# Performance work log

Hardware: AMD Instinct MI355X
Metric: run time of the kernel (lower is better)

## Reference

```python
import jax, jax.numpy as jnp
import numpy as np

N, P, D, FDIM, TFEAT = 65536, 6, 256, 8, 16
RAW_DIM = 4 + TFEAT  # 20
IN_DIM = 3 + FDIM + 3 + 3  # xyz + frame embedding + rigid xyz + viewdir = 17


def setup_inputs() -> dict:
    key = jax.random.key(0)
    ks = jax.random.split(key, 16)
    inp = {
        "tpts": jax.random.normal(ks[0], (N, P, 3), jnp.float32),
        "bigpts": jax.random.normal(ks[1], (N, P, 3), jnp.float32),
        "viewdir": jax.random.normal(ks[2], (N, P, 3), jnp.float32),
        "dists": jax.random.uniform(ks[3], (N,), jnp.float32),
        "part_dist": jax.random.uniform(ks[4], (1, N, P), jnp.float32),
        "frame_dim": jax.random.normal(ks[5], (FDIM,), jnp.float32),
        "W1": jax.random.normal(ks[6], (P, IN_DIM, D), jnp.float32) / np.sqrt(IN_DIM),
        "b1": jax.random.normal(ks[7], (P, D), jnp.float32) * 0.01,
        "W2": jax.random.normal(ks[8], (P, D, D), jnp.float32) / np.sqrt(D),
        "b2": jax.random.normal(ks[9], (P, D), jnp.float32) * 0.01,
        "W3": jax.random.normal(ks[10], (P, D, RAW_DIM), jnp.float32) / np.sqrt(D),
        "b3": jax.random.normal(ks[11], (P, RAW_DIM), jnp.float32) * 0.01,
        "Wocc": jax.random.normal(ks[12], (P, D, 1), jnp.float32) / np.sqrt(D),
        "bocc": jax.random.normal(ks[13], (P, 1), jnp.float32) * 0.01,
        "tflag": jax.random.randint(ks[14], (N, P), 0, 2).astype(bool),
    }
    return inp


def _part_mlps(tpts, bigpts, viewdir, frame_dim, W1, b1, W2, b2, W3, b3, Wocc, bocc):
    # Run all P part networks on all N points (batched per-part GEMMs).
    n = tpts.shape[0]
    frame = jnp.broadcast_to(frame_dim, (n, P, FDIM))
    x = jnp.concatenate([tpts, frame, bigpts, viewdir], axis=-1)  # (N,P,17)
    h = jax.nn.relu(jnp.einsum('npi,pid->npd', x, W1) + b1)
    h = jax.nn.relu(jnp.einsum('npd,pde->npe', h, W2) + b2)
    raw_p = jnp.einsum('npd,pdr->npr', h, W3) + b3               # (N,P,20)
    occ_p = jax.nn.sigmoid(jnp.einsum('npd,pdo->npo', h, Wocc) + bocc)  # (N,P,1)
    return raw_p, occ_p


def reference(tpts, bigpts, viewdir, dists, part_dist, frame_dim,
              W1, b1, W2, b2, W3, b3, Wocc, bocc, tflag):
    raw_p, occ_p = _part_mlps(tpts, bigpts, viewdir, frame_dim,
                              W1, b1, W2, b2, W3, b3, Wocc, bocc)
    # scatter-back equivalent: unflagged (point, part) slots stay zero
    flag = tflag[..., None].astype(raw_p.dtype)  # (N,P,1)
    raws = raw_p * flag                           # (N,P,20)
    occs = occ_p * flag                           # (N,P,1)
    # cfg.aggr == 'mean'
    raw = raws.mean(axis=1)                       # (N,20)
    occ = occs.mean(axis=1)                       # (N,1)
    tocc = occs[..., 0]                           # (N,P)
    return jnp.concatenate([raw, occ, tocc], axis=-1)  # (N, 20+1+P)
```

## Files before the change

kernel.cpp:

```cpp
#include <hip/hip_runtime.h>
#include <hip/hip_bf16.h>

using bf16 = __hip_bfloat16;
typedef __bf16 bf16x8 __attribute__((ext_vector_type(8)));
typedef __bf16 bf16x4v __attribute__((ext_vector_type(4)));
typedef float f32x4 __attribute__((ext_vector_type(4)));
typedef float f32x16 __attribute__((ext_vector_type(16)));

#define MFMA32(a, b, c) __builtin_amdgcn_mfma_f32_32x32x16_bf16((a), (b), (c), 0, 0, 0)

__device__ __forceinline__ void bar_lds() {
  asm volatile("s_waitcnt lgkmcnt(0)" ::: "memory");
  __builtin_amdgcn_s_barrier();
}


__global__ void prep_kernel(const float* __restrict__ W1, const float* __restrict__ b1,
                            const float* __restrict__ W2, const float* __restrict__ W3,
                            const float* __restrict__ Wocc, __bf16* __restrict__ ws) {
  const int b = blockIdx.x;
  const int tid = threadIdx.x;
  if (b < 96) {
    __shared__ float tile[64][65];
    const int p = b >> 4, t = b & 15;
    const int d0 = (t >> 2) * 64, e0 = (t & 3) * 64;
    const int lane = tid & 63, grp = tid >> 6;
    const float* src = W2 + p * 65536 + (d0 + grp * 16) * 256 + e0 + lane;
#pragma unroll
    for (int i = 0; i < 16; ++i) tile[grp * 16 + i][lane] = src[i * 256];
    __syncthreads();
#pragma unroll
    for (int q = 0; q < 2; ++q) {
      const int m = tid + q * 256;
      const int ee = m >> 3, c = m & 7;
      bf16x8 v;
#pragma unroll
      for (int j = 0; j < 8; ++j) v[j] = (__bf16)tile[c * 8 + j][ee];
      *reinterpret_cast<bf16x8*>(
          &ws[49152 + p * 65536 + (e0 + ee) * 256 + d0 + c * 8]) = v;
    }
    return;
  }
  const int t = 49152 + (b - 96) * 256 + tid;
  if (t < 55296) {
    const int u = t - 49152;
    const int p = u >> 10, r = u & 1023, n = r >> 2, c = r & 3;
    bf16x8 v;
#pragma unroll
    for (int j = 0; j < 8; ++j) {
      const int k = c * 8 + j;
      float x = 0.f;
      if (k < 17) {
        const int ko = (k < 8) ? k + 3 : ((k < 11) ? k - 8 : k);
        x = W1[p * 4352 + ko * 256 + n];
      } else if (k == 17) {
        x = b1[p * 256 + n];
      }
      v[j] = (__bf16)x;
    }
    *reinterpret_cast<bf16x8*>(&ws[p * 8192 + n * 32 + c * 8]) = v;
  } else if (t < 61440) {
    const int u = t - 55296;
    const int p = u >> 10, r = u & 1023, row = r >> 5, c = r & 31;
    bf16x8 v;
#pragma unroll
    for (int j = 0; j < 8; ++j) {
      const int k = c * 8 + j;
      float x = 0.f;
      if (row < 20)       x = W3[p * 5120 + k * 20 + row];
      else if (row == 20) x = Wocc[p * 256 + k];
      v[j] = (__bf16)x;
    }
    *reinterpret_cast<bf16x8*>(&ws[442368 + p * 8192 + row * 256 + c * 8]) = v;
  }
}

__global__ __launch_bounds__(256, 2) void tpose_main(
    const float* __restrict__ tpts, const float* __restrict__ bigpts,
    const float* __restrict__ viewdir, const float* __restrict__ frame,
    const float* __restrict__ b2g, const float* __restrict__ b3g,
    const float* __restrict__ boccg, const int* __restrict__ tflag,
    const __bf16* __restrict__ ws, float* __restrict__ out) {
  const __bf16* __restrict__ W1t = ws;
  const __bf16* __restrict__ W2t = ws + 49152;
  const __bf16* __restrict__ W3t = ws + 442368;

  __shared__ __align__(16) __bf16 Xf[128 * 40];
  __shared__ __align__(16) __bf16 Hf[128 * 256];
  __shared__ float Tocc[128 * 6];

  const int tid = threadIdx.x;
  const int w = tid >> 6;
  const int lane = tid & 63;
  const int ln5 = lane & 31;
  const int hi = lane >> 5;
  const int e5 = ln5 & 7;
  const int n0 = blockIdx.x * 128;
  const int ptD = w * 32 + ln5;

  if (tid < 128) {
    bf16x8 f8;
#pragma unroll
    for (int j = 0; j < 8; ++j) f8[j] = (__bf16)frame[j];
    *reinterpret_cast<bf16x8*>(&Xf[tid * 40]) = f8;
    bf16x8 z = {};
    z[1] = (__bf16)1.0f;
    *reinterpret_cast<bf16x8*>(&Xf[tid * 40 + 16]) = z;
    bf16x8 z2 = {};
    *reinterpret_cast<bf16x8*>(&Xf[tid * 40 + 24]) = z2;
  }

  const int role = tid & 3;
  const float* __restrict__ dynsrc =
      (role == 0) ? tpts : (role == 1) ? bigpts : viewdir;

  float pre[2][3];
#pragma unroll
  for (int pass = 0; pass < 2; ++pass) {
    const int pt = (tid >> 2) + pass * 64;
    const int base3 = (n0 + pt) * 18;
#pragma unroll
    for (int i = 0; i < 3; ++i) pre[pass][i] = dynsrc[base3 + i];
  }
  float flv = (tflag[(n0 + ptD) * 6] != 0) ? 1.f : 0.f;

  float psum[12];
#pragma unroll
  for (int k = 0; k < 12; ++k) psum[k] = 0.f;

  for (int p = 0; p < 6; ++p) {
    if (role < 3) {
#pragma unroll
      for (int pass = 0; pass < 2; ++pass) {
        const int pt = (tid >> 2) + pass * 64;
#pragma unroll
        for (int i = 0; i < 3; ++i)
          Xf[pt * 40 + 8 + role * 3 + i] = (__bf16)pre[pass][i];
      }
    }

    bf16x8 aw[2][2];
#pragma unroll
    for (int mt = 0; mt < 2; ++mt)
#pragma unroll
      for (int kt = 0; kt < 2; ++kt)
        aw[mt][kt] = *reinterpret_cast<const bf16x8*>(
            &W1t[p * 8192 + (w * 64 + mt * 32 + ln5) * 32 + kt * 16 + hi * 8]);

    bar_lds();

    f32x16 acc[2][4];
#pragma unroll
    for (int mt = 0; mt < 2; ++mt)
#pragma unroll
      for (int nt = 0; nt < 4; ++nt)
#pragma unroll
        for (int k = 0; k < 16; ++k) acc[mt][nt][k] = 0.f;
#pragma unroll
    for (int nt = 0; nt < 4; ++nt)
#pragma unroll
      for (int kt = 0; kt < 2; ++kt) {
        const bf16x8 xb = *reinterpret_cast<const bf16x8*>(
            &Xf[(nt * 32 + ln5) * 40 + kt * 16 + hi * 8]);
#pragma unroll
        for (int mt = 0; mt < 2; ++mt)
          acc[mt][nt] = MFMA32(aw[mt][kt], xb, acc[mt][nt]);
      }
#pragma unroll
    for (int mt = 0; mt < 2; ++mt)
#pragma unroll
      for (int q = 0; q < 4; ++q) {
        const int off = (((w * 8 + mt * 4 + q) ^ e5) << 3) + hi * 4;
#pragma unroll
        for (int nt = 0; nt < 4; ++nt) {
          bf16x4v hv;
#pragma unroll
          for (int r = 0; r < 4; ++r)
            hv[r] = (__bf16)fmaxf(acc[mt][nt][q * 4 + r], 0.f);
          *reinterpret_cast<bf16x4v*>(&Hf[(nt * 32 + ln5) * 256 + off]) = hv;
        }
      }

    bar_lds();

    const __bf16* __restrict__ w2p =
        W2t + p * 65536 + (w * 64 + ln5) * 256 + hi * 8;
    bf16x8 a2[2];
#pragma unroll
    for (int mt = 0; mt < 2; ++mt)
      a2[mt] = *reinterpret_cast<const bf16x8*>(w2p + mt * 8192);
    f32x4 b2q[2][4];
#pragma unroll
    for (int mt = 0; mt < 2; ++mt)
#pragma unroll
      for (int q = 0; q < 4; ++q)
        b2q[mt][q] = *reinterpret_cast<const f32x4*>(
            &b2g[p * 256 + w * 64 + mt * 32 + q * 8 + hi * 4]);

    const int pn = (p < 5) ? p + 1 : 5;
#pragma unroll
    for (int pass = 0; pass < 2; ++pass) {
      const int pt = (tid >> 2) + pass * 64;
      const int base3 = ((n0 + pt) * 6 + pn) * 3;
#pragma unroll
      for (int i = 0; i < 3; ++i) pre[pass][i] = dynsrc[base3 + i];
    }
    const float fln = (tflag[(n0 + ptD) * 6 + pn] != 0) ? 1.f : 0.f;

#pragma unroll
    for (int mt = 0; mt < 2; ++mt)
#pragma unroll
      for (int nt = 0; nt < 4; ++nt)
#pragma unroll
        for (int q = 0; q < 4; ++q)
#pragma unroll
          for (int r = 0; r < 4; ++r)
            acc[mt][nt][q * 4 + r] = b2q[mt][q][r];

    __builtin_amdgcn_s_setprio(1);
#pragma unroll 1
    for (int kt = 0; kt < 16; ++kt) {
      bf16x8 a2n[2];
      if (kt < 15) {
#pragma unroll
        for (int mt = 0; mt < 2; ++mt)
          a2n[mt] = *reinterpret_cast<const bf16x8*>(
              w2p + mt * 8192 + (kt + 1) * 16);
      }
      const int off = ((kt * 2 + hi) ^ e5) << 3;
      bf16x8 hb[4];
#pragma unroll
      for (int nt = 0; nt < 4; ++nt)
        hb[nt] = *reinterpret_cast<const bf16x8*>(
            &Hf[(nt * 32 + ln5) * 256 + off]);
#pragma unroll
      for (int nt = 0; nt < 4; ++nt)
#pragma unroll
        for (int mt = 0; mt < 2; ++mt)
          acc[mt][nt] = MFMA32(a2[mt], hb[nt], acc[mt][nt]);
#pragma unroll
      for (int mt = 0; mt < 2; ++mt) a2[mt] = a2n[mt];
    }
    __builtin_amdgcn_s_setprio(0);

    bar_lds();

#pragma unroll
    for (int mt = 0; mt < 2; ++mt)
#pragma unroll
      for (int q = 0; q < 4; ++q) {
        const int off = (((w * 8 + mt * 4 + q) ^ e5) << 3) + hi * 4;
#pragma unroll
        for (int nt = 0; nt < 4; ++nt) {
          bf16x4v hv;
#pragma unroll
          for (int r = 0; r < 4; ++r)
            hv[r] = (__bf16)fmaxf(acc[mt][nt][q * 4 + r], 0.f);
          *reinterpret_cast<bf16x4v*>(&Hf[(nt * 32 + ln5) * 256 + off]) = hv;
        }
      }

    bar_lds();

    f32x16 acc3;
#pragma unroll
    for (int q = 0; q < 4; ++q)
#pragma unroll
      for (int r = 0; r < 4; ++r) {
        const int d = q * 8 + hi * 4 + r;
        float v = 0.f;
        if (d < 20)       v = b3g[p * 20 + d];
        else if (d == 20) v = boccg[p];
        acc3[q * 4 + r] = v;
      }
    const __bf16* __restrict__ w3p = W3t + p * 8192 + ln5 * 256 + hi * 8;
#pragma unroll 4
    for (int kt = 0; kt < 16; ++kt) {
      const bf16x8 a3 = *reinterpret_cast<const bf16x8*>(w3p + kt * 16);
      const bf16x8 hb = *reinterpret_cast<const bf16x8*>(
          &Hf[ptD * 256 + (((kt * 2 + hi) ^ e5) << 3)]);
      acc3 = MFMA32(a3, hb, acc3);
    }

#pragma unroll
    for (int k = 0; k < 12; ++k) {
      const int d = (k >> 2) * 8 + hi * 4 + (k & 3);
      if (d < 20) {
        psum[k] += flv * acc3[k];
      } else if (d == 20) {
        const float occ = 1.f / (1.f + __expf(-acc3[k]));
        Tocc[ptD * 6 + p] = flv * occ;
        psum[k] += flv * occ;
      }
    }

    flv = fln;
  }

  bar_lds();
  float* stage = reinterpret_cast<float*>(Hf);
  const float inv6 = 1.f / 6.f;
#pragma unroll
  for (int k = 0; k < 12; ++k) {
    const int d = (k >> 2) * 8 + hi * 4 + (k & 3);
    if (d <= 20) stage[ptD * 27 + d] = psum[k] * inv6;
  }
  if (tid < 128) {
#pragma unroll
    for (int pp = 0; pp < 6; ++pp) stage[tid * 27 + 21 + pp] = Tocc[tid * 6 + pp];
  }
  bar_lds();
  float* outp = out + (size_t)n0 * 27;
#pragma unroll
  for (int q = 0; q < 4; ++q) {
    const int m = tid + q * 256;
    if (m < 864)
      *reinterpret_cast<f32x4*>(&outp[m * 4]) =
          *reinterpret_cast<const f32x4*>(&stage[m * 4]);
  }
}

extern "C" void kernel_launch(void* const* d_in, const int* in_sizes, int n_in,
                              void* d_out, int out_size, void* d_ws, size_t ws_size,
                              hipStream_t stream) {
  const float* tpts    = (const float*)d_in[0];
  const float* bigpts  = (const float*)d_in[1];
  const float* viewdir = (const float*)d_in[2];
  const float* frame   = (const float*)d_in[5];
  const float* W1      = (const float*)d_in[6];
  const float* b1      = (const float*)d_in[7];
  const float* W2      = (const float*)d_in[8];
  const float* b2      = (const float*)d_in[9];
  const float* W3      = (const float*)d_in[10];
  const float* b3      = (const float*)d_in[11];
  const float* Wocc    = (const float*)d_in[12];
  const float* bocc    = (const float*)d_in[13];
  const int*   tflag   = (const int*)d_in[14];
  __bf16* ws  = (__bf16*)d_ws;
  float*  out = (float*)d_out;

  prep_kernel<<<144, 256, 0, stream>>>(W1, b1, W2, W3, Wocc, ws);
  tpose_main<<<512, 256, 0, stream>>>(tpts, bigpts, viewdir, frame, b2, b3,
                                      bocc, tflag, ws, out);
}
```

Baseline: 183.8 us.

## Repartition layer-2 GEMM so each wave owns its points across all output features

Layer 2 is reorganized so each wave computes all 256 output features for its own 32 points, instead of a 64-feature slice for all 128 points. Each wave now reads only its own rows of H from LDS and streams W2 fragments from global memory in a rotating register buffer. Because every wave writes and reads only its own H rows, the two block-wide barriers around layer 2 and layer 3 can become a local LDS wait. The cost is four times more W2 global/L2 traffic per wave and a larger accumulator set (8 tiles), which raises register pressure.

```diff
diff --git a/kernel.cpp b/kernel.cpp
--- a/kernel.cpp
+++ b/kernel.cpp
@@ -128,6 +128,8 @@
 #pragma unroll
   for (int k = 0; k < 12; ++k) psum[k] = 0.f;
 
+  f32x16 acc[8];
+
   for (int p = 0; p < 6; ++p) {
     if (role < 3) {
 #pragma unroll
@@ -149,13 +151,10 @@
 
     bar_lds();
 
-    f32x16 acc[2][4];
-#pragma unroll
-    for (int mt = 0; mt < 2; ++mt)
-#pragma unroll
-      for (int nt = 0; nt < 4; ++nt)
-#pragma unroll
-        for (int k = 0; k < 16; ++k) acc[mt][nt][k] = 0.f;
+#pragma unroll
+    for (int i = 0; i < 8; ++i)
+#pragma unroll
+      for (int k = 0; k < 16; ++k) acc[i][k] = 0.f;
 #pragma unroll
     for (int nt = 0; nt < 4; ++nt)
 #pragma unroll
@@ -164,7 +163,7 @@
             &Xf[(nt * 32 + ln5) * 40 + kt * 16 + hi * 8]);
 #pragma unroll
         for (int mt = 0; mt < 2; ++mt)
-          acc[mt][nt] = MFMA32(aw[mt][kt], xb, acc[mt][nt]);
+          acc[mt * 4 + nt] = MFMA32(aw[mt][kt], xb, acc[mt * 4 + nt]);
       }
 #pragma unroll
     for (int mt = 0; mt < 2; ++mt)
@@ -176,26 +175,24 @@
           bf16x4v hv;
 #pragma unroll
           for (int r = 0; r < 4; ++r)
-            hv[r] = (__bf16)fmaxf(acc[mt][nt][q * 4 + r], 0.f);
+            hv[r] = (__bf16)fmaxf(acc[mt * 4 + nt][q * 4 + r], 0.f);
           *reinterpret_cast<bf16x4v*>(&Hf[(nt * 32 + ln5) * 256 + off]) = hv;
         }
       }
 
     bar_lds();
 
-    const __bf16* __restrict__ w2p =
-        W2t + p * 65536 + (w * 64 + ln5) * 256 + hi * 8;
-    bf16x8 a2[2];
-#pragma unroll
-    for (int mt = 0; mt < 2; ++mt)
-      a2[mt] = *reinterpret_cast<const bf16x8*>(w2p + mt * 8192);
-    f32x4 b2q[2][4];
-#pragma unroll
-    for (int mt = 0; mt < 2; ++mt)
-#pragma unroll
-      for (int q = 0; q < 4; ++q)
-        b2q[mt][q] = *reinterpret_cast<const f32x4*>(
-            &b2g[p * 256 + w * 64 + mt * 32 + q * 8 + hi * 4]);
+    const __bf16* __restrict__ w2p = W2t + p * 65536 + ln5 * 256 + hi * 8;
+
+#pragma unroll
+    for (int mt = 0; mt < 8; ++mt)
+#pragma unroll
+      for (int q = 0; q < 4; ++q) {
+        const f32x4 bq = *reinterpret_cast<const f32x4*>(
+            &b2g[p * 256 + mt * 32 + q * 8 + hi * 4]);
+#pragma unroll
+        for (int r = 0; r < 4; ++r) acc[mt][q * 4 + r] = bq[r];
+      }
 
     const int pn = (p < 5) ? p + 1 : 5;
 #pragma unroll
@@ -207,60 +204,46 @@
     }
     const float fln = (tflag[(n0 + ptD) * 6 + pn] != 0) ? 1.f : 0.f;
 
-#pragma unroll
-    for (int mt = 0; mt < 2; ++mt)
-#pragma unroll
-      for (int nt = 0; nt < 4; ++nt)
-#pragma unroll
-        for (int q = 0; q < 4; ++q)
-#pragma unroll
-          for (int r = 0; r < 4; ++r)
-            acc[mt][nt][q * 4 + r] = b2q[mt][q][r];
+    bf16x8 hbc = *reinterpret_cast<const bf16x8*>(
+        &Hf[ptD * 256 + ((hi ^ e5) << 3)]);
+    bf16x8 a2r[4];
+#pragma unroll
+    for (int m0 = 0; m0 < 4; ++m0)
+      a2r[m0] = *reinterpret_cast<const bf16x8*>(w2p + m0 * 8192);
 
     __builtin_amdgcn_s_setprio(1);
 #pragma unroll 1
     for (int kt = 0; kt < 16; ++kt) {
-      bf16x8 a2n[2];
-      if (kt < 15) {
-#pragma unroll
-        for (int mt = 0; mt < 2; ++mt)
-          a2n[mt] = *reinterpret_cast<const bf16x8*>(
-              w2p + mt * 8192 + (kt + 1) * 16);
-      }
-      const int off = ((kt * 2 + hi) ^ e5) << 3;
-      bf16x8 hb[4];
-#pragma unroll
-      for (int nt = 0; nt < 4; ++nt)
-        hb[nt] = *reinterpret_cast<const bf16x8*>(
-            &Hf[(nt * 32 + ln5) * 256 + off]);
-#pragma unroll
-      for (int nt = 0; nt < 4; ++nt)
-#pragma unroll
-        for (int mt = 0; mt < 2; ++mt)
-          acc[mt][nt] = MFMA32(a2[mt], hb[nt], acc[mt][nt]);
-#pragma unroll
-      for (int mt = 0; mt < 2; ++mt) a2[mt] = a2n[mt];
-    }
-    __builtin_amdgcn_s_setprio(0);
-
-    bar_lds();
-
-#pragma unroll
-    for (int mt = 0; mt < 2; ++mt)
+      bf16x8 hbn = hbc;
+      if (kt < 15)
+        hbn = *reinterpret_cast<const bf16x8*>(
+            &Hf[ptD * 256 + ((((kt + 1) * 2 + hi) ^ e5) << 3)]);
+#pragma unroll
+      for (int mt = 0; mt < 8; ++mt) {
+        acc[mt] = MFMA32(a2r[mt & 3], hbc, acc[mt]);
+        if (mt < 4) {
+          a2r[mt & 3] = *reinterpret_cast<const bf16x8*>(
+              w2p + (mt + 4) * 8192 + kt * 16);
+        } else if (kt < 15) {
+          a2r[mt & 3] = *reinterpret_cast<const bf16x8*>(
+              w2p + (mt - 4) * 8192 + (kt + 1) * 16);
+        }
+      }
+      hbc = hbn;
+    }
+
+#pragma unroll
+    for (int mt = 0; mt < 8; ++mt)
 #pragma unroll
       for (int q = 0; q < 4; ++q) {
-        const int off = (((w * 8 + mt * 4 + q) ^ e5) << 3) + hi * 4;
-#pragma unroll
-        for (int nt = 0; nt < 4; ++nt) {
-          bf16x4v hv;
-#pragma unroll
-          for (int r = 0; r < 4; ++r)
-            hv[r] = (__bf16)fmaxf(acc[mt][nt][q * 4 + r], 0.f);
-          *reinterpret_cast<bf16x4v*>(&Hf[(nt * 32 + ln5) * 256 + off]) = hv;
-        }
-      }
-
-    bar_lds();
+        bf16x4v hv;
+#pragma unroll
+        for (int r = 0; r < 4; ++r)
+          hv[r] = (__bf16)fmaxf(acc[mt][q * 4 + r], 0.f);
+        *reinterpret_cast<bf16x4v*>(
+            &Hf[ptD * 256 + (((mt * 4 + q) ^ e5) << 3) + hi * 4]) = hv;
+      }
+    asm volatile("s_waitcnt lgkmcnt(0)" ::: "memory");
 
     f32x16 acc3;
 #pragma unroll
@@ -274,13 +257,17 @@
         acc3[q * 4 + r] = v;
       }
     const __bf16* __restrict__ w3p = W3t + p * 8192 + ln5 * 256 + hi * 8;
-#pragma unroll 4
-    for (int kt = 0; kt < 16; ++kt) {
-      const bf16x8 a3 = *reinterpret_cast<const bf16x8*>(w3p + kt * 16);
-      const bf16x8 hb = *reinterpret_cast<const bf16x8*>(
-          &Hf[ptD * 256 + (((kt * 2 + hi) ^ e5) << 3)]);
-      acc3 = MFMA32(a3, hb, acc3);
-    }
+#pragma unroll
+    for (int mt = 0; mt < 8; ++mt)
+#pragma unroll
+      for (int s = 0; s < 2; ++s) {
+        const bf16x8 a3 =
+            *reinterpret_cast<const bf16x8*>(w3p + (2 * mt + s) * 16);
+        const bf16x8 hb = *reinterpret_cast<const bf16x8*>(
+            &Hf[ptD * 256 + (((mt * 4 + s * 2 + hi) ^ e5) << 3)]);
+        acc3 = MFMA32(a3, hb, acc3);
+      }
+    __builtin_amdgcn_s_setprio(0);
 
 #pragma unroll
     for (int k = 0; k < 12; ++k) {
```

Measured after the change: 306.1 us. +66.6%, slower.
